# Kernel optimization log

Measured on AMD Instinct MI355X. Metric: run time of the kernel, lower is better.

Reference implementation:

```python
import jax, jax.numpy as jnp
from jax import lax
import numpy as np

NPOINT = 1024   # S: number of sampled centroids
NSAMPLE = 32    # K: neighbors per centroid (unmasked ball query = k-nearest via argsort)


def _gather(p, i):
    # p: [B,N,C], i: [B,...] int -> [B,...,C]
    return jax.vmap(lambda pb, ib: pb[ib])(p, i)


def _fps(xyz, farthest_init, npoint):
    # Iterative farthest point sampling, faithful to the torch loop.
    B, N, _ = xyz.shape
    dist0 = jnp.full((B, N), 1e10, dtype=xyz.dtype)

    def step(carry, _):
        distance, farthest = carry
        centroid = jnp.take_along_axis(xyz, farthest[:, None, None], axis=1)  # [B,1,3]
        d = jnp.sum((xyz - centroid) ** 2, -1)          # [B,N]
        distance = jnp.minimum(distance, d)
        return (distance, jnp.argmax(distance, -1)), farthest

    _, cent = lax.scan(step, (dist0, farthest_init.astype(jnp.int32)), None, length=npoint)
    return cent.T  # [B, npoint]


def _sq_dist(src, dst):
    # src: [B,S,3], dst: [B,N,3] -> [B,S,N]
    return (jnp.sum(src ** 2, -1)[:, :, None]
            + jnp.sum(dst ** 2, -1)[:, None, :]
            - 2.0 * jnp.einsum('bsc,bnc->bsn', src, dst))


def setup_inputs() -> dict:
    key = jax.random.key(0)
    ks = jax.random.split(key, 6)
    B, N, C = 8, 4096, 6
    inp = {
        'xyz': jax.random.normal(ks[0], (B, N, 3), jnp.float32),
        'points': jax.random.normal(ks[1], (B, N, C), jnp.float32),
        'farthest_init': jax.random.randint(ks[2], (B,), 0, N),
    }
    dims = [C + 3, 64, 64, 128]
    for li in range(3):
        inp[f'w{li}'] = jax.random.normal(ks[3 + li], (dims[li + 1], dims[li]), jnp.float32) * 0.1
        inp[f'b{li}'] = jnp.zeros((dims[li + 1],), jnp.float32)
    return inp


def reference(xyz, points, farthest_init, w0, b0, w1, b1, w2, b2):
    fps_idx = _fps(xyz, farthest_init, NPOINT)            # [B,S]
    new_xyz = _gather(xyz, fps_idx)                       # [B,S,3]
    dist = _sq_dist(new_xyz, xyz)                         # [B,S,N]
    _, idx = lax.top_k(-dist, NSAMPLE)                    # k-nearest == argsort[:, :, :K]
    g_xyz = _gather(xyz, idx) - new_xyz[:, :, None, :]    # [B,S,K,3]
    g_pts = _gather(points, idx)                          # [B,S,K,C]
    h = jnp.concatenate([g_xyz, g_pts], axis=-1)          # [B,S,K,C+3]
    for w, b in ((w0, b0), (w1, b1), (w2, b2)):           # 1x1 conv MLP + relu
        h = jax.nn.relu(jnp.einsum('bskc,oc->bsko', h, w) + b)
    new_points = jnp.max(h, axis=2)                       # max-pool over K -> [B,S,128]
    return new_xyz, new_points
```

## Files before the change

### kernel.cpp

```cpp
#include <hip/hip_runtime.h>

#define INF_F 3.402823466e+38f
typedef unsigned long long u64;
typedef __attribute__((ext_vector_type(2))) float f32x2;

__device__ __forceinline__ float f_add(float a, float b){ return __fadd_rn(a,b); }
__device__ __forceinline__ float f_sub(float a, float b){ return __fsub_rn(a,b); }
__device__ __forceinline__ float f_mul(float a, float b){ return __fmul_rn(a,b); }

__device__ __forceinline__ f32x2 pk_add(f32x2 a, f32x2 b){ f32x2 d; asm("v_pk_add_f32 %0, %1, %2" : "=v"(d) : "v"(a), "v"(b)); return d; }
__device__ __forceinline__ f32x2 pk_mul(f32x2 a, f32x2 b){ f32x2 d; asm("v_pk_mul_f32 %0, %1, %2" : "=v"(d) : "v"(a), "v"(b)); return d; }
__device__ __forceinline__ f32x2 pk_fma(f32x2 a, f32x2 b, f32x2 c){ f32x2 d; asm("v_pk_fma_f32 %0, %1, %2, %3" : "=v"(d) : "v"(a), "v"(b), "v"(c)); return d; }

template<int CTRL>
__device__ __forceinline__ double dpp_d(double x) {
    u64 u = (u64)__double_as_longlong(x);
    int lo = __builtin_amdgcn_update_dpp(0, (int)(unsigned)u,        CTRL, 0xF, 0xF, true);
    int hi = __builtin_amdgcn_update_dpp(0, (int)(unsigned)(u>>32), CTRL, 0xF, 0xF, true);
    return __longlong_as_double((long long)(((u64)(unsigned)hi << 32) | (unsigned)lo));
}
template<int CTRL>
__device__ __forceinline__ float dpp_f(float x) {
    int r = __builtin_amdgcn_update_dpp(0, __float_as_int(x), CTRL, 0xF, 0xF, true);
    return __int_as_float(r);
}
__device__ __forceinline__ float swz16_f(float x) {
    return __int_as_float(__builtin_amdgcn_ds_swizzle(__float_as_int(x), 0x401F));
}
__device__ __forceinline__ double readlane_d(double x, int l) {
    u64 u = (u64)__double_as_longlong(x);
    int lo = __builtin_amdgcn_readlane((int)(unsigned)u,        l);
    int hi = __builtin_amdgcn_readlane((int)(unsigned)(u>>32), l);
    return __longlong_as_double((long long)(((u64)(unsigned)hi << 32) | (unsigned)lo));
}
__device__ __forceinline__ double pack_key(float nd, unsigned low) {
    return __longlong_as_double((long long)(((u64)__float_as_uint(nd) << 32) | (u64)low));
}

__device__ __forceinline__ double wave_max_key(double k) {
    k = fmax(k, dpp_d<0xB1>(k));
    k = fmax(k, dpp_d<0x4E>(k));
    k = fmax(k, dpp_d<0x141>(k));
    k = fmax(k, dpp_d<0x140>(k));
    double a = readlane_d(k, 0),  b = readlane_d(k, 16);
    double c = readlane_d(k, 32), d = readlane_d(k, 48);
    return fmax(fmax(a, b), fmax(c, d));
}
__device__ __forceinline__ double wave_min_key(double k) {
    k = fmin(k, dpp_d<0xB1>(k));
    k = fmin(k, dpp_d<0x4E>(k));
    k = fmin(k, dpp_d<0x141>(k));
    k = fmin(k, dpp_d<0x140>(k));
    double a = readlane_d(k, 0),  b = readlane_d(k, 16);
    double c = readlane_d(k, 32), d = readlane_d(k, 48);
    return fmin(fmin(a, b), fmin(c, d));
}

__global__ __launch_bounds__(256, 1) void fps_kernel(
    const float* __restrict__ xyz, const int* __restrict__ farthest_init,
    float* __restrict__ out_new_xyz)
{
    const int b    = blockIdx.x;
    const int tid  = threadIdx.x;
    const int lane = tid & 63;
    const int wid  = tid >> 6;

    __shared__ float4 sp[4096];
    __shared__ int    hist[1024];
    __shared__ double red[2][4];

    const float* xb = xyz + (size_t)b * 4096 * 3;
    for (int n = tid; n < 4096; n += 256)
        sp[n] = make_float4(xb[n*3+0], xb[n*3+1], xb[n*3+2], 0.0f);
    __syncthreads();

    f32x2 px[8], py[8], pz[8], dist2[8];
    #pragma unroll
    for (int jp = 0; jp < 8; ++jp) {
        const int n0 = (2*jp) * 256 + tid, n1 = n0 + 256;
        float4 a = sp[n0], c = sp[n1];
        px[jp] = (f32x2){a.x, c.x};
        py[jp] = (f32x2){a.y, c.y};
        pz[jp] = (f32x2){a.z, c.z};
        dist2[jp] = (f32x2){1e10f, 1e10f};
    }
    const unsigned lowbase = 4095u - (unsigned)tid;

    int far = farthest_init[b];
    float4 cen = sp[far];
    float cx = cen.x, cy = cen.y, cz = cen.z;
    int p = 0;
    #pragma unroll 1
    for (int it = 0; it < 1024; ++it) {
        if (tid == 0) hist[it] = far;
        const f32x2 ncx = (f32x2){-cx, -cx};
        const f32x2 ncy = (f32x2){-cy, -cy};
        const f32x2 ncz = (f32x2){-cz, -cz};

        double a0 = -1.0, a1 = -1.0, a2 = -1.0, a3 = -1.0;
        #pragma unroll
        for (int jp = 0; jp < 8; ++jp) {
            f32x2 dx = pk_add(px[jp], ncx);
            f32x2 dy = pk_add(py[jp], ncy);
            f32x2 dz = pk_add(pz[jp], ncz);
            f32x2 d2 = pk_add(pk_add(pk_mul(dx,dx), pk_mul(dy,dy)), pk_mul(dz,dz));
            float nd0 = fminf(dist2[jp][0], d2[0]); dist2[jp][0] = nd0;
            float nd1 = fminf(dist2[jp][1], d2[1]); dist2[jp][1] = nd1;
            double k0 = pack_key(nd0, lowbase - (unsigned)((2*jp)*256));
            double k1 = pack_key(nd1, lowbase - (unsigned)((2*jp+1)*256));
            if (jp & 1) { a2 = fmax(a2, k0); a3 = fmax(a3, k1); }
            else        { a0 = fmax(a0, k0); a1 = fmax(a1, k1); }
        }
        double wkey = wave_max_key(fmax(fmax(a0, a1), fmax(a2, a3)));
        if (lane == 0) red[p][wid] = wkey;
        __syncthreads();
        const double g = fmax(fmax(red[p][0], red[p][1]),
                              fmax(red[p][2], red[p][3]));
        far = 4095 - (int)(unsigned)((u64)__double_as_longlong(g) & 0xFFFFFFFFull);
        float4 cc = sp[far];
        cx = cc.x; cy = cc.y; cz = cc.z;
        p ^= 1;
    }
    __syncthreads();
    #pragma unroll
    for (int q = 0; q < 4; ++q) {
        int s  = q * 256 + tid;
        float4 cc = sp[hist[s]];
        float* o = out_new_xyz + ((size_t)b * 1024 + s) * 3;
        o[0] = cc.x; o[1] = cc.y; o[2] = cc.z;
    }
}

template<int G>
__device__ __forceinline__ double rebuild8(const double (&key)[64], double w) {
    const double DINF = __builtin_huge_val();
    double m = DINF;
    #pragma unroll
    for (int e = 0; e < 8; ++e) {
        double v = key[G*8+e];
        v = (v > w) ? v : DINF;
        m = fmin(m, v);
    }
    return m;
}

__global__ __launch_bounds__(256, 1) void knn_kernel(
    const float* __restrict__ xyz, const float* __restrict__ new_xyz,
    int* __restrict__ out_idx)
{
    const int tid  = threadIdx.x;
    const int lane = tid & 63;
    const int wid  = tid >> 6;
    const int blk  = blockIdx.x * 4 + wid;
    const int b    = blk >> 10;

    const float* xb = xyz + (size_t)b * 4096 * 3;
    const float* cp = new_xyz + (size_t)blk * 3;
    const float cx = cp[0], cy = cp[1], cz = cp[2];
    const float src2 = f_add(f_add(f_mul(cx,cx), f_mul(cy,cy)), f_mul(cz,cz));

    double key[64];
    #pragma unroll
    for (int j = 0; j < 64; ++j) {
        const int n = j * 64 + lane;
        const float* pt = xb + n * 3;
        float x = pt[0], y = pt[1], z = pt[2];
        float dst2 = f_add(f_add(f_mul(x,x), f_mul(y,y)), f_mul(z,z));
        float dot  = f_add(f_add(f_mul(cx,x), f_mul(cy,y)), f_mul(cz,z));
        float d = f_sub(f_add(src2, dst2), f_mul(2.0f, dot));
        key[j] = __longlong_as_double((long long)(((u64)__float_as_uint(d) << 32) | (u64)(unsigned)n));
    }

    double gm[8];
    #pragma unroll
    for (int g = 0; g < 8; ++g) {
        double m = key[g*8];
        #pragma unroll
        for (int e = 1; e < 8; ++e) m = fmin(m, key[g*8+e]);
        gm[g] = m;
    }

    double w = -1.0;
    int myidx = 0;
    #pragma unroll 1
    for (int t = 0; t < 32; ++t) {
        double lm = fmin(fmin(fmin(gm[0], gm[1]), fmin(gm[2], gm[3])),
                         fmin(fmin(gm[4], gm[5]), fmin(gm[6], gm[7])));
        double gmin = wave_min_key(lm);
        int n = (int)(unsigned)((u64)__double_as_longlong(gmin) & 0xFFFFFFFFull);
        if (lane == t) myidx = n;
        w = gmin;
        const int gs = __builtin_amdgcn_readfirstlane(n >> 9);
        switch (gs) {
            case 0: gm[0] = rebuild8<0>(key, w); break;
            case 1: gm[1] = rebuild8<1>(key, w); break;
            case 2: gm[2] = rebuild8<2>(key, w); break;
            case 3: gm[3] = rebuild8<3>(key, w); break;
            case 4: gm[4] = rebuild8<4>(key, w); break;
            case 5: gm[5] = rebuild8<5>(key, w); break;
            case 6: gm[6] = rebuild8<6>(key, w); break;
            case 7: gm[7] = rebuild8<7>(key, w); break;
        }
    }
    if (lane < 32) out_idx[(size_t)blk * 32 + lane] = myidx;
}

__global__ __launch_bounds__(256, 1) void mlp_kernel(
    const float* __restrict__ xyz, const float* __restrict__ points,
    const int* __restrict__ knn_idx,
    const float* __restrict__ w0, const float* __restrict__ b0,
    const float* __restrict__ w1, const float* __restrict__ b1,
    const float* __restrict__ w2, const float* __restrict__ b2,
    const float* __restrict__ new_xyz, float* __restrict__ out_np)
{
    const int tid = threadIdx.x;
    const int k   = tid & 31;
    const int gs  = blockIdx.x * 8 + (tid >> 5);
    const int b   = gs >> 10;
    const int n   = knn_idx[(size_t)gs * 32 + k];

    const float cx = new_xyz[gs*3+0], cy = new_xyz[gs*3+1], cz = new_xyz[gs*3+2];
    const float* pxyz = xyz + ((size_t)b * 4096 + n) * 3;
    float h0[9];
    h0[0] = pxyz[0] - cx;
    h0[1] = pxyz[1] - cy;
    h0[2] = pxyz[2] - cz;
    const float* pp = points + ((size_t)b * 4096 + n) * 6;
    #pragma unroll
    for (int c = 0; c < 6; ++c) h0[3 + c] = pp[c];

    f32x2 h1p[32];
    #pragma unroll
    for (int o = 0; o < 64; o += 2) {
        float accA = b0[o], accB = b0[o+1];
        #pragma unroll
        for (int c = 0; c < 9; ++c) {
            accA = fmaf(h0[c], w0[o*9+c],     accA);
            accB = fmaf(h0[c], w0[(o+1)*9+c], accB);
        }
        h1p[o>>1] = (f32x2){fmaxf(accA, 0.0f), fmaxf(accB, 0.0f)};
    }

    const f32x2* w1v = (const f32x2*)w1;
    f32x2 h2p[32];
    #pragma unroll
    for (int o = 0; o < 64; o += 2) {
        f32x2 accA = (f32x2){b1[o],   0.0f};
        f32x2 accB = (f32x2){b1[o+1], 0.0f};
        #pragma unroll
        for (int i = 0; i < 32; ++i) {
            accA = pk_fma(h1p[i], w1v[o*32+i],     accA);
            accB = pk_fma(h1p[i], w1v[(o+1)*32+i], accB);
        }
        h2p[o>>1] = (f32x2){fmaxf(accA[0]+accA[1], 0.0f), fmaxf(accB[0]+accB[1], 0.0f)};
    }

    const f32x2* w2v = (const f32x2*)w2;
    float* outp = out_np + (size_t)gs * 128;
    for (int og = 0; og < 4; ++og) {
        float keep = 0.0f;
        for (int o2 = 0; o2 < 32; ++o2) {
            const int o = og * 32 + o2;
            f32x2 acc = (f32x2){b2[o], 0.0f};
            #pragma unroll
            for (int i = 0; i < 32; ++i) acc = pk_fma(h2p[i], w2v[o*32+i], acc);
            float m = fmaxf(acc[0] + acc[1], 0.0f);
            m = fmaxf(m, dpp_f<0xB1>(m));
            m = fmaxf(m, dpp_f<0x4E>(m));
            m = fmaxf(m, dpp_f<0x141>(m));
            m = fmaxf(m, dpp_f<0x140>(m));
            m = fmaxf(m, swz16_f(m));
            keep = (k == o2) ? m : keep;
        }
        outp[og * 32 + k] = keep;
    }
}

__global__ __launch_bounds__(256) void knn_mlp_kernel(
    const float* __restrict__ xyz, const float* __restrict__ points,
    const float* __restrict__ w0, const float* __restrict__ b0,
    const float* __restrict__ w1, const float* __restrict__ b1,
    const float* __restrict__ w2, const float* __restrict__ b2,
    const float* __restrict__ new_xyz, float* __restrict__ out_np)
{
    const int blk    = blockIdx.x;
    const int b      = blk >> 7;
    const int s_base = (blk & 127) * 8;
    const int tid    = threadIdx.x;
    const int lane   = tid & 63;
    const int wid    = tid >> 6;

    __shared__ float sx[4096], sy[4096], sz[4096];
    __shared__ float cent[8][3];
    __shared__ int   idxbuf[8][32];

    const float* xb = xyz + (size_t)b * 4096 * 3;
    for (int n = tid; n < 4096; n += 256) {
        sx[n] = xb[n*3+0]; sy[n] = xb[n*3+1]; sz[n] = xb[n*3+2];
    }
    if (tid < 24) ((float*)cent)[tid] = new_xyz[((size_t)b * 1024 + s_base) * 3 + tid];
    __syncthreads();

    for (int si = 0; si < 2; ++si) {
        const int sl = wid * 2 + si;
        const float cx = cent[sl][0], cy = cent[sl][1], cz = cent[sl][2];
        const float src2 = f_add(f_add(f_mul(cx,cx), f_mul(cy,cy)), f_mul(cz,cz));
        float d[64];
        #pragma unroll
        for (int j = 0; j < 64; ++j) {
            int n = j * 64 + lane;
            float x = sx[n], y = sy[n], z = sz[n];
            float dst2 = f_add(f_add(f_mul(x,x), f_mul(y,y)), f_mul(z,z));
            float dot  = f_add(f_add(f_mul(cx,x), f_mul(cy,y)), f_mul(cz,z));
            d[j] = f_sub(f_add(src2, dst2), f_mul(2.0f, dot));
        }
        int myg  = 0;
        int prev = -1;
        for (int t = 0; t < 32; ++t) {
            float bv = INF_F; int bi = 0x7fffffff;
            #pragma unroll
            for (int j = 0; j < 64; ++j) {
                int n = j * 64 + lane;
                if (n == prev) d[j] = INF_F;
                float v = d[j];
                if (v < bv) { bv = v; bi = n; }
            }
            #pragma unroll
            for (int m = 1; m < 64; m <<= 1) {
                float ov = __shfl_xor(bv, m);
                int   oi = __shfl_xor(bi, m);
                if (ov < bv || (ov == bv && oi < bi)) { bv = ov; bi = oi; }
            }
            if (lane == t) myg = bi;
            prev = bi;
        }
        if (lane < 32) idxbuf[sl][lane] = myg;
    }
    __syncthreads();

    const int k   = tid & 31;
    const int sl2 = tid >> 5;
    const int s   = s_base + sl2;
    const int n   = idxbuf[sl2][k];

    const float cx = cent[sl2][0], cy = cent[sl2][1], cz = cent[sl2][2];
    float h0[9];
    h0[0] = sx[n] - cx;
    h0[1] = sy[n] - cy;
    h0[2] = sz[n] - cz;
    const float* pp = points + ((size_t)b * 4096 + n) * 6;
    #pragma unroll
    for (int c = 0; c < 6; ++c) h0[3 + c] = pp[c];

    float h1[64];
    #pragma unroll
    for (int o = 0; o < 64; ++o) {
        float acc = b0[o];
        #pragma unroll
        for (int c = 0; c < 9; ++c) acc = fmaf(h0[c], w0[o*9+c], acc);
        h1[o] = fmaxf(acc, 0.0f);
    }
    float h2[64];
    #pragma unroll
    for (int o = 0; o < 64; ++o) {
        float acc = b1[o];
        #pragma unroll
        for (int c = 0; c < 64; ++c) acc = fmaf(h1[c], w1[o*64+c], acc);
        h2[o] = fmaxf(acc, 0.0f);
    }
    float* outp = out_np + ((size_t)b * 1024 + s) * 128;
    for (int og = 0; og < 4; ++og) {
        float keep = 0.0f;
        for (int o2 = 0; o2 < 32; ++o2) {
            const int o = og * 32 + o2;
            float acc = b2[o];
            #pragma unroll
            for (int c = 0; c < 64; ++c) acc = fmaf(h2[c], w2[o*64+c], acc);
            float m = fmaxf(acc, 0.0f);
            #pragma unroll
            for (int mm = 1; mm < 32; mm <<= 1)
                m = fmaxf(m, __shfl_xor(m, mm));
            keep = (k == o2) ? m : keep;
        }
        outp[og * 32 + k] = keep;
    }
}

extern "C" void kernel_launch(void* const* d_in, const int* in_sizes, int n_in,
                              void* d_out, int out_size, void* d_ws, size_t ws_size,
                              hipStream_t stream) {
    const float* xyz           = (const float*)d_in[0];
    const float* points        = (const float*)d_in[1];
    const int*   farthest_init = (const int*)  d_in[2];
    const float* w0 = (const float*)d_in[3];
    const float* b0 = (const float*)d_in[4];
    const float* w1 = (const float*)d_in[5];
    const float* b1 = (const float*)d_in[6];
    const float* w2 = (const float*)d_in[7];
    const float* b2 = (const float*)d_in[8];

    float* out        = (float*)d_out;
    float* new_xyz    = out;
    float* new_points = out + 8 * 1024 * 3;

    fps_kernel<<<8, 256, 0, stream>>>(xyz, farthest_init, new_xyz);

    if (ws_size >= (size_t)(8192 * 32 * sizeof(int))) {
        int* knn_idx = (int*)d_ws;
        knn_kernel<<<2048, 256, 0, stream>>>(xyz, new_xyz, knn_idx);
        mlp_kernel<<<1024, 256, 0, stream>>>(xyz, points, knn_idx,
                                             w0, b0, w1, b1, w2, b2,
                                             new_xyz, new_points);
    } else {
        knn_mlp_kernel<<<1024, 256, 0, stream>>>(xyz, points, w0, b0, w1, b1, w2, b2,
                                                 new_xyz, new_points);
    }
}
```

Before: 781.0 us.

## Widen FPS block to 16 waves and carry winner coordinates through reduction

The farthest point sampling kernel now runs 1024 threads per batch instead of 256, so each thread holds 4 points instead of 16, which shortens the serial per-iteration distance update. Each wave reads its winning point's coordinates straight from registers via readlane and publishes key plus xyz to shared memory. A 16-lane DPP argmax then picks the global winner, which removes the dependent LDS lookup of the centroid after the barrier. The cost is a barrier across 16 waves per iteration and a longer cross-wave reduction, while the grid stays at only 8 blocks.

```diff
diff --git a/kernel.cpp b/kernel.cpp
--- a/kernel.cpp
+++ b/kernel.cpp
@@ -32,6 +32,12 @@
     int lo = __builtin_amdgcn_readlane((int)(unsigned)u,        l);
     int hi = __builtin_amdgcn_readlane((int)(unsigned)(u>>32), l);
     return __longlong_as_double((long long)(((u64)(unsigned)hi << 32) | (unsigned)lo));
+}
+__device__ __forceinline__ float readlane_f(float x, int l) {
+    return __int_as_float(__builtin_amdgcn_readlane(__float_as_int(x), l));
+}
+__device__ __forceinline__ unsigned key_lo(double k) {
+    return (unsigned)((u64)__double_as_longlong(k) & 0xFFFFFFFFull);
 }
 __device__ __forceinline__ double pack_key(float nd, unsigned low) {
     return __longlong_as_double((long long)(((u64)__float_as_uint(nd) << 32) | (u64)low));
@@ -56,7 +62,7 @@
     return fmin(fmin(a, b), fmin(c, d));
 }
 
-__global__ __launch_bounds__(256, 1) void fps_kernel(
+__global__ __launch_bounds__(1024, 1) void fps16_kernel(
     const float* __restrict__ xyz, const int* __restrict__ farthest_init,
     float* __restrict__ out_new_xyz)
 {
@@ -67,29 +73,31 @@
 
     __shared__ float4 sp[4096];
     __shared__ int    hist[1024];
-    __shared__ double red[2][4];
+    __shared__ float4 slotA[2][16];
+    __shared__ float  slotB[2][16];
 
     const float* xb = xyz + (size_t)b * 4096 * 3;
-    for (int n = tid; n < 4096; n += 256)
+    for (int n = tid; n < 4096; n += 1024)
         sp[n] = make_float4(xb[n*3+0], xb[n*3+1], xb[n*3+2], 0.0f);
     __syncthreads();
 
-    f32x2 px[8], py[8], pz[8], dist2[8];
-    #pragma unroll
-    for (int jp = 0; jp < 8; ++jp) {
-        const int n0 = (2*jp) * 256 + tid, n1 = n0 + 256;
+    f32x2 px[2], py[2], pz[2], d2a[2];
+    #pragma unroll
+    for (int jp = 0; jp < 2; ++jp) {
+        const int n0 = (2*jp)*1024 + tid, n1 = n0 + 1024;
         float4 a = sp[n0], c = sp[n1];
         px[jp] = (f32x2){a.x, c.x};
         py[jp] = (f32x2){a.y, c.y};
         pz[jp] = (f32x2){a.z, c.z};
-        dist2[jp] = (f32x2){1e10f, 1e10f};
-    }
-    const unsigned lowbase = 4095u - (unsigned)tid;
+        d2a[jp] = (f32x2){1e10f, 1e10f};
+    }
+    const unsigned low0 = 4095u - (unsigned)tid;
 
     int far = farthest_init[b];
     float4 cen = sp[far];
     float cx = cen.x, cy = cen.y, cz = cen.z;
     int p = 0;
+
     #pragma unroll 1
     for (int it = 0; it < 1024; ++it) {
         if (tid == 0) hist[it] = far;
@@ -97,36 +105,84 @@
         const f32x2 ncy = (f32x2){-cy, -cy};
         const f32x2 ncz = (f32x2){-cz, -cz};
 
-        double a0 = -1.0, a1 = -1.0, a2 = -1.0, a3 = -1.0;
-        #pragma unroll
-        for (int jp = 0; jp < 8; ++jp) {
-            f32x2 dx = pk_add(px[jp], ncx);
-            f32x2 dy = pk_add(py[jp], ncy);
-            f32x2 dz = pk_add(pz[jp], ncz);
+        f32x2 nd01, nd23;
+        {
+            f32x2 dx = pk_add(px[0], ncx);
+            f32x2 dy = pk_add(py[0], ncy);
+            f32x2 dz = pk_add(pz[0], ncz);
             f32x2 d2 = pk_add(pk_add(pk_mul(dx,dx), pk_mul(dy,dy)), pk_mul(dz,dz));
-            float nd0 = fminf(dist2[jp][0], d2[0]); dist2[jp][0] = nd0;
-            float nd1 = fminf(dist2[jp][1], d2[1]); dist2[jp][1] = nd1;
-            double k0 = pack_key(nd0, lowbase - (unsigned)((2*jp)*256));
-            double k1 = pack_key(nd1, lowbase - (unsigned)((2*jp+1)*256));
-            if (jp & 1) { a2 = fmax(a2, k0); a3 = fmax(a3, k1); }
-            else        { a0 = fmax(a0, k0); a1 = fmax(a1, k1); }
-        }
-        double wkey = wave_max_key(fmax(fmax(a0, a1), fmax(a2, a3)));
-        if (lane == 0) red[p][wid] = wkey;
+            nd01[0] = fminf(d2a[0][0], d2[0]);
+            nd01[1] = fminf(d2a[0][1], d2[1]);
+            d2a[0] = nd01;
+        }
+        {
+            f32x2 dx = pk_add(px[1], ncx);
+            f32x2 dy = pk_add(py[1], ncy);
+            f32x2 dz = pk_add(pz[1], ncz);
+            f32x2 d2 = pk_add(pk_add(pk_mul(dx,dx), pk_mul(dy,dy)), pk_mul(dz,dz));
+            nd23[0] = fminf(d2a[1][0], d2[0]);
+            nd23[1] = fminf(d2a[1][1], d2[1]);
+            d2a[1] = nd23;
+        }
+        double k0 = pack_key(nd01[0], low0);
+        double k1 = pack_key(nd01[1], low0 - 1024u);
+        double k2 = pack_key(nd23[0], low0 - 2048u);
+        double k3 = pack_key(nd23[1], low0 - 3072u);
+        double best = fmax(fmax(k0, k1), fmax(k2, k3));
+
+        double wkey = wave_max_key(best);
+        const int n_w = 4095 - (int)key_lo(wkey);
+        const int jsel  = __builtin_amdgcn_readfirstlane(n_w >> 10);
+        const int olane = __builtin_amdgcn_readfirstlane(n_w & 63);
+        f32x2 xa = (jsel & 2) ? px[1] : px[0];
+        f32x2 ya = (jsel & 2) ? py[1] : py[0];
+        f32x2 za = (jsel & 2) ? pz[1] : pz[0];
+        float xs = (jsel & 1) ? xa[1] : xa[0];
+        float ys = (jsel & 1) ? ya[1] : ya[0];
+        float zs = (jsel & 1) ? za[1] : za[0];
+        const float xw = readlane_f(xs, olane);
+        const float yw = readlane_f(ys, olane);
+        const float zw = readlane_f(zs, olane);
+
+        if (lane == 0) {
+            u64 kb = (u64)__double_as_longlong(wkey);
+            slotA[p][wid] = make_float4(__uint_as_float((unsigned)kb),
+                                        __uint_as_float((unsigned)(kb >> 32)), xw, yw);
+            slotB[p][wid] = zw;
+        }
         __syncthreads();
-        const double g = fmax(fmax(red[p][0], red[p][1]),
-                              fmax(red[p][2], red[p][3]));
-        far = 4095 - (int)(unsigned)((u64)__double_as_longlong(g) & 0xFFFFFFFFull);
-        float4 cc = sp[far];
-        cx = cc.x; cy = cc.y; cz = cc.z;
+
+        double kf; float xf, yf, zf;
+        if (lane < 16) {
+            float4 a = slotA[p][lane];
+            kf = __longlong_as_double((long long)(
+                     ((u64)__float_as_uint(a.y) << 32) | (u64)__float_as_uint(a.x)));
+            xf = a.z; yf = a.w; zf = slotB[p][lane];
+        } else {
+            kf = -1.0; xf = 0.0f; yf = 0.0f; zf = 0.0f;
+        }
+        {
+            double pk; float pxx, pyy, pzz; bool gt;
+            pk = dpp_d<0xB1>(kf); pxx = dpp_f<0xB1>(xf); pyy = dpp_f<0xB1>(yf); pzz = dpp_f<0xB1>(zf);
+            gt = pk > kf; kf = gt ? pk : kf; xf = gt ? pxx : xf; yf = gt ? pyy : yf; zf = gt ? pzz : zf;
+            pk = dpp_d<0x4E>(kf); pxx = dpp_f<0x4E>(xf); pyy = dpp_f<0x4E>(yf); pzz = dpp_f<0x4E>(zf);
+            gt = pk > kf; kf = gt ? pk : kf; xf = gt ? pxx : xf; yf = gt ? pyy : yf; zf = gt ? pzz : zf;
+            pk = dpp_d<0x141>(kf); pxx = dpp_f<0x141>(xf); pyy = dpp_f<0x141>(yf); pzz = dpp_f<0x141>(zf);
+            gt = pk > kf; kf = gt ? pk : kf; xf = gt ? pxx : xf; yf = gt ? pyy : yf; zf = gt ? pzz : zf;
+            pk = dpp_d<0x140>(kf); pxx = dpp_f<0x140>(xf); pyy = dpp_f<0x140>(yf); pzz = dpp_f<0x140>(zf);
+            gt = pk > kf; kf = gt ? pk : kf; xf = gt ? pxx : xf; yf = gt ? pyy : yf; zf = gt ? pzz : zf;
+        }
+        const double gkey = readlane_d(kf, 0);
+        cx = readlane_f(xf, 0);
+        cy = readlane_f(yf, 0);
+        cz = readlane_f(zf, 0);
+        far = 4095 - (int)key_lo(gkey);
         p ^= 1;
     }
     __syncthreads();
-    #pragma unroll
-    for (int q = 0; q < 4; ++q) {
-        int s  = q * 256 + tid;
-        float4 cc = sp[hist[s]];
-        float* o = out_new_xyz + ((size_t)b * 1024 + s) * 3;
+    {
+        float4 cc = sp[hist[tid]];
+        float* o = out_new_xyz + ((size_t)b * 1024 + tid) * 3;
         o[0] = cc.x; o[1] = cc.y; o[2] = cc.z;
     }
 }
@@ -403,7 +459,7 @@
     float* new_xyz    = out;
     float* new_points = out + 8 * 1024 * 3;
 
-    fps_kernel<<<8, 256, 0, stream>>>(xyz, farthest_init, new_xyz);
+    fps16_kernel<<<8, 1024, 0, stream>>>(xyz, farthest_init, new_xyz);
 
     if (ws_size >= (size_t)(8192 * 32 * sizeof(int))) {
         int* knn_idx = (int*)d_ws;
```

New measurement: 1.429 ms. 83.0% more time.

## Widen FPS to 512 threads and reduce float max before key packing

Applied to the files above, without the earlier changes.

The farthest-point-sampling kernel now runs 512 threads per batch instead of 256, so each thread holds 8 points instead of 16. The per-thread argmax first takes a float max, then picks the smallest index among ties, and packs a single 64-bit key, instead of packing and max-reducing a double key per point. This shortens the serial per-iteration latency of the 1024-step loop. The cost is eight waves taking part in each block barrier and the cross-wave reduction.

```diff
diff --git a/kernel.cpp b/kernel.cpp
--- a/kernel.cpp
+++ b/kernel.cpp
@@ -32,6 +32,9 @@
     int lo = __builtin_amdgcn_readlane((int)(unsigned)u,        l);
     int hi = __builtin_amdgcn_readlane((int)(unsigned)(u>>32), l);
     return __longlong_as_double((long long)(((u64)(unsigned)hi << 32) | (unsigned)lo));
+}
+__device__ __forceinline__ unsigned key_lo(double k) {
+    return (unsigned)((u64)__double_as_longlong(k) & 0xFFFFFFFFull);
 }
 __device__ __forceinline__ double pack_key(float nd, unsigned low) {
     return __longlong_as_double((long long)(((u64)__float_as_uint(nd) << 32) | (u64)low));
@@ -56,7 +59,7 @@
     return fmin(fmin(a, b), fmin(c, d));
 }
 
-__global__ __launch_bounds__(256, 1) void fps_kernel(
+__global__ __launch_bounds__(512, 1) void fps8_kernel(
     const float* __restrict__ xyz, const int* __restrict__ farthest_init,
     float* __restrict__ out_new_xyz)
 {
@@ -67,29 +70,29 @@
 
     __shared__ float4 sp[4096];
     __shared__ int    hist[1024];
-    __shared__ double red[2][4];
+    __shared__ double red[2][8];
 
     const float* xb = xyz + (size_t)b * 4096 * 3;
-    for (int n = tid; n < 4096; n += 256)
+    for (int n = tid; n < 4096; n += 512)
         sp[n] = make_float4(xb[n*3+0], xb[n*3+1], xb[n*3+2], 0.0f);
     __syncthreads();
 
-    f32x2 px[8], py[8], pz[8], dist2[8];
-    #pragma unroll
-    for (int jp = 0; jp < 8; ++jp) {
-        const int n0 = (2*jp) * 256 + tid, n1 = n0 + 256;
+    f32x2 px[4], py[4], pz[4], d2a[4];
+    #pragma unroll
+    for (int jp = 0; jp < 4; ++jp) {
+        const int n0 = (2*jp)*512 + tid, n1 = n0 + 512;
         float4 a = sp[n0], c = sp[n1];
         px[jp] = (f32x2){a.x, c.x};
         py[jp] = (f32x2){a.y, c.y};
         pz[jp] = (f32x2){a.z, c.z};
-        dist2[jp] = (f32x2){1e10f, 1e10f};
-    }
-    const unsigned lowbase = 4095u - (unsigned)tid;
+        d2a[jp] = (f32x2){1e10f, 1e10f};
+    }
 
     int far = farthest_init[b];
     float4 cen = sp[far];
     float cx = cen.x, cy = cen.y, cz = cen.z;
     int p = 0;
+
     #pragma unroll 1
     for (int it = 0; it < 1024; ++it) {
         if (tid == 0) hist[it] = far;
@@ -97,34 +100,41 @@
         const f32x2 ncy = (f32x2){-cy, -cy};
         const f32x2 ncz = (f32x2){-cz, -cz};
 
-        double a0 = -1.0, a1 = -1.0, a2 = -1.0, a3 = -1.0;
-        #pragma unroll
-        for (int jp = 0; jp < 8; ++jp) {
+        float nd[8];
+        #pragma unroll
+        for (int jp = 0; jp < 4; ++jp) {
             f32x2 dx = pk_add(px[jp], ncx);
             f32x2 dy = pk_add(py[jp], ncy);
             f32x2 dz = pk_add(pz[jp], ncz);
             f32x2 d2 = pk_add(pk_add(pk_mul(dx,dx), pk_mul(dy,dy)), pk_mul(dz,dz));
-            float nd0 = fminf(dist2[jp][0], d2[0]); dist2[jp][0] = nd0;
-            float nd1 = fminf(dist2[jp][1], d2[1]); dist2[jp][1] = nd1;
-            double k0 = pack_key(nd0, lowbase - (unsigned)((2*jp)*256));
-            double k1 = pack_key(nd1, lowbase - (unsigned)((2*jp+1)*256));
-            if (jp & 1) { a2 = fmax(a2, k0); a3 = fmax(a3, k1); }
-            else        { a0 = fmax(a0, k0); a1 = fmax(a1, k1); }
-        }
-        double wkey = wave_max_key(fmax(fmax(a0, a1), fmax(a2, a3)));
+            float a0 = fminf(d2a[jp][0], d2[0]);
+            float a1 = fminf(d2a[jp][1], d2[1]);
+            d2a[jp][0] = a0; d2a[jp][1] = a1;
+            nd[2*jp+0] = a0;
+            nd[2*jp+1] = a1;
+        }
+        float vmax = fmaxf(fmaxf(fmaxf(nd[0], nd[1]), fmaxf(nd[2], nd[3])),
+                           fmaxf(fmaxf(nd[4], nd[5]), fmaxf(nd[6], nd[7])));
+        unsigned bestn = 0xFFFFFFFFu;
+        #pragma unroll
+        for (int j = 0; j < 8; ++j) {
+            unsigned nj = (unsigned)(j*512 + tid);
+            bestn = min(bestn, (nd[j] == vmax) ? nj : 0xFFFFFFFFu);
+        }
+        double wkey = wave_max_key(pack_key(vmax, 4095u - bestn));
         if (lane == 0) red[p][wid] = wkey;
         __syncthreads();
-        const double g = fmax(fmax(red[p][0], red[p][1]),
-                              fmax(red[p][2], red[p][3]));
-        far = 4095 - (int)(unsigned)((u64)__double_as_longlong(g) & 0xFFFFFFFFull);
+        const double g = fmax(fmax(fmax(red[p][0], red[p][1]), fmax(red[p][2], red[p][3])),
+                              fmax(fmax(red[p][4], red[p][5]), fmax(red[p][6], red[p][7])));
+        far = 4095 - (int)key_lo(g);
         float4 cc = sp[far];
         cx = cc.x; cy = cc.y; cz = cc.z;
         p ^= 1;
     }
     __syncthreads();
     #pragma unroll
-    for (int q = 0; q < 4; ++q) {
-        int s  = q * 256 + tid;
+    for (int q = 0; q < 2; ++q) {
+        int s = q * 512 + tid;
         float4 cc = sp[hist[s]];
         float* o = out_new_xyz + ((size_t)b * 1024 + s) * 3;
         o[0] = cc.x; o[1] = cc.y; o[2] = cc.z;
@@ -403,7 +413,7 @@
     float* new_xyz    = out;
     float* new_points = out + 8 * 1024 * 3;
 
-    fps_kernel<<<8, 256, 0, stream>>>(xyz, farthest_init, new_xyz);
+    fps8_kernel<<<8, 512, 0, stream>>>(xyz, farthest_init, new_xyz);
 
     if (ws_size >= (size_t)(8192 * 32 * sizeof(int))) {
         int* knn_idx = (int*)d_ws;
```

Result: slower. 881.2 us (+12.8%).
